# Performance work log

Measured on AMD Instinct MI355X. Metric: run time of the kernel, lower is better.

The kernel has to match this reference:

```python
import jax, jax.numpy as jnp
import numpy as np

EPS = 1e-6
B, T, J, D, H = 8, 512, 26, 256, 8
DH = D // H
HID = 4 * D


def logmap0(x):
    # x: [..., d+1] on hyperboloid (curvature -1). Tangent at origin -> [..., d]
    x0 = jnp.clip(x[..., :1], 1.0 + 1e-7, None)
    xs = x[..., 1:]
    n = jnp.maximum(jnp.linalg.norm(xs, axis=-1, keepdims=True), EPS)
    return jnp.arccosh(x0) * xs / n


def expmap0(v):
    # v: [..., d] tangent at origin -> [..., d+1] on hyperboloid
    n = jnp.maximum(jnp.linalg.norm(v, axis=-1, keepdims=True), EPS)
    return jnp.concatenate([jnp.cosh(n), jnp.sinh(n) * v / n], axis=-1)


def layernorm(v, g, b):
    m = jnp.mean(v, axis=-1, keepdims=True)
    var = jnp.var(v, axis=-1, keepdims=True)
    return (v - m) * jax.lax.rsqrt(var + 1e-5) * g + b


def lorentz_residual(x, z):
    # Lorentz centroid: normalize x+z so <m,m>_L = -1
    m = x + z
    mink = -m[..., :1] ** 2 + jnp.sum(m[..., 1:] ** 2, axis=-1, keepdims=True)
    return m / jnp.sqrt(jnp.clip(-mink, EPS, None))


def setup_inputs() -> dict:
    key = jax.random.key(0)
    ks = jax.random.split(key, 12)
    xs = jax.random.normal(ks[0], (B, T, J, D), jnp.float32) * 0.5
    x0 = jnp.sqrt(1.0 + jnp.sum(xs ** 2, axis=-1, keepdims=True))
    x = jnp.concatenate([x0, xs], axis=-1)  # valid points on H^d
    s = 1.0 / np.sqrt(D)
    inp = {
        "x": x,
        "g1": jnp.ones((D,), jnp.float32), "beta1": jnp.zeros((D,), jnp.float32),
        "Wq": jax.random.normal(ks[1], (D, D), jnp.float32) * s,
        "Wk": jax.random.normal(ks[2], (D, D), jnp.float32) * s,
        "Wv": jax.random.normal(ks[3], (D, D), jnp.float32) * s,
        "Wo": jax.random.normal(ks[4], (D, D), jnp.float32) * s,
        "bq": jnp.zeros((D,), jnp.float32), "bk": jnp.zeros((D,), jnp.float32),
        "bv": jnp.zeros((D,), jnp.float32), "bo": jnp.zeros((D,), jnp.float32),
        "g2": jnp.ones((D,), jnp.float32), "beta2": jnp.zeros((D,), jnp.float32),
        "W1": jax.random.normal(ks[5], (D, HID), jnp.float32) * s,
        "bf1": jnp.zeros((HID,), jnp.float32),
        "W2": jax.random.normal(ks[6], (HID, D), jnp.float32) * (1.0 / np.sqrt(HID)),
        "bf2": jnp.zeros((D,), jnp.float32),
    }
    return inp


def reference(x, g1, beta1, Wq, Wk, Wv, Wo, bq, bk, bv, bo, g2, beta2, W1, bf1, W2, bf2):
    # norm1: tangent-space LayerNorm
    u = layernorm(logmap0(x), g1, beta1)            # [B,T,J,D]
    xn = expmap0(u)
    # linear temporal attention (per joint, across T)
    t = logmap0(xn)
    q = (t @ Wq + bq).reshape(B, T, J, H, DH)
    k = (t @ Wk + bk).reshape(B, T, J, H, DH)
    v = (t @ Wv + bv).reshape(B, T, J, H, DH)
    pq = jax.nn.elu(q) + 1.0
    pk = jax.nn.elu(k) + 1.0
    kv = jnp.einsum('btjhk,btjhd->bjhkd', pk, v)    # O(T) global context
    ksum = jnp.sum(pk, axis=1)                      # [B,J,H,DH]
    num = jnp.einsum('btjhk,bjhkd->btjhd', pq, kv)
    den = jnp.einsum('btjhk,bjhk->btjh', pq, ksum)[..., None] + EPS
    o = (num / den).reshape(B, T, J, D) @ Wo + bo
    z = expmap0(o)
    # Lorentz (Minkowski) residual
    h = lorentz_residual(x, z)
    # norm2 + FFN in tangent space
    u2 = layernorm(logmap0(h), g2, beta2)
    f = jax.nn.gelu(u2 @ W1 + bf1) @ W2 + bf2
    return expmap0(f)
```

## Files before the change

### kernel.cpp

```cpp
#include <hip/hip_runtime.h>
#include <hip/hip_bf16.h>
#include <math.h>


#define EPSF 1e-6f
#define B_ 8
#define T_ 512
#define J_ 26
#define D_ 256
#define H_ 8
#define DH_ 32
#define HID_ 1024
#define NP1 257
#define R_ (B_*T_*J_)

typedef float  f32x4  __attribute__((ext_vector_type(4)));
typedef short  s16x8  __attribute__((ext_vector_type(8)));
typedef short  s16x4  __attribute__((ext_vector_type(4)));

__device__ __forceinline__ void async16(const void* g, void* l) {
  __builtin_amdgcn_global_load_lds(
      (const __attribute__((address_space(1))) unsigned int*)g,
      (__attribute__((address_space(3))) unsigned int*)l, 16, 0, 0);
}

__device__ __forceinline__ float wave_sum(float v) {
#pragma unroll
  for (int m = 32; m; m >>= 1) v += __shfl_xor(v, m, 64);
  return v;
}

__global__ __launch_bounds__(256) void k_wconv(const float* __restrict__ W,
                                               __hip_bfloat16* __restrict__ Wt,
                                               int K, int N) {
  __shared__ float tile[32][33];
  int n0 = blockIdx.x * 32, k0 = blockIdx.y * 32;
  int tx = threadIdx.x, ty = threadIdx.y;
#pragma unroll
  for (int i = ty; i < 32; i += 8) tile[i][tx] = W[(size_t)(k0 + i) * N + n0 + tx];
  __syncthreads();
#pragma unroll
  for (int i = ty; i < 32; i += 8)
    Wt[(size_t)(n0 + i) * K + k0 + tx] = __float2bfloat16(tile[tx][i]);
}

__global__ __launch_bounds__(256) void k_t(const float* __restrict__ x,
                                           const float* __restrict__ g1,
                                           const float* __restrict__ beta1,
                                           __hip_bfloat16* __restrict__ t) {
  int r = blockIdx.x * 4 + (threadIdx.x >> 6);
  int l = threadIdx.x & 63;
  const float* xr = x + (size_t)r * NP1;
  float xs[4];
#pragma unroll
  for (int i = 0; i < 4; ++i) xs[i] = xr[1 + l + 64*i];
  float p1 = xs[0]+xs[1]+xs[2]+xs[3];
  float p2 = xs[0]*xs[0]+xs[1]*xs[1]+xs[2]*xs[2]+xs[3]*xs[3];
  float s1 = wave_sum(p1);
  float s2 = wave_sum(p2);
  float mean = s1 * (1.0f/256.0f);
  float var = s2 * (1.0f/256.0f) - mean*mean;
  float rstd = rsqrtf(var + 1e-5f);
#pragma unroll
  for (int i = 0; i < 4; ++i) {
    int c = l + 64*i;
    t[(size_t)r * D_ + c] = __float2bfloat16((xs[i]-mean)*rstd*g1[c] + beta1[c]);
  }
}

#define PHASE(BUF, MH, NH, GIDX, DO_VM) {                                      \
    s16x8 af_[4][2]; s16x8 bf_[2][2];                                          \
    const char* ab_ = lds + ((BUF)*2+(MH))*16384;                              \
    const char* bb_ = lds + 65536 + ((BUF)*2+(NH))*16384;                      \
    _Pragma("unroll") for (int f_ = 0; f_ < 4; ++f_)                           \
      _Pragma("unroll") for (int ks_ = 0; ks_ < 2; ++ks_)                      \
        af_[f_][ks_] = *(const s16x8*)(ab_ + aoffs[f_][ks_]);                  \
    _Pragma("unroll") for (int ni_ = 0; ni_ < 2; ++ni_)                        \
      _Pragma("unroll") for (int ks_ = 0; ks_ < 2; ++ks_)                      \
        bf_[ni_][ks_] = *(const s16x8*)(bb_ + boffs[ni_][ks_]);                \
    STAGE_HALF((GIDX) + 6);                                                    \
    if (DO_VM) asm volatile("s_waitcnt vmcnt(4)" ::: "memory");                \
    asm volatile("s_barrier" ::: "memory");                                    \
    __builtin_amdgcn_sched_barrier(0);                                         \
    __builtin_amdgcn_s_setprio(1);                                             \
    _Pragma("unroll") for (int ks_ = 0; ks_ < 2; ++ks_)                        \
      _Pragma("unroll") for (int f_ = 0; f_ < 4; ++f_)                         \
        _Pragma("unroll") for (int ni_ = 0; ni_ < 2; ++ni_)                    \
          acc[(MH)*4+f_][(NH)*2+ni_] = __builtin_amdgcn_mfma_f32_16x16x32_bf16(\
              bf_[ni_][ks_], af_[f_][ks_], acc[(MH)*4+f_][(NH)*2+ni_], 0,0,0); \
    __builtin_amdgcn_s_setprio(0);                                             \
    asm volatile("s_barrier" ::: "memory");                                    \
  }

template<int ACT, int OUTF, int KDIM>
__global__ __launch_bounds__(512, 2) void k_gemm(const __hip_bfloat16* __restrict__ A,
                                                 const __hip_bfloat16* __restrict__ Bt,
                                                 const float* __restrict__ bias,
                                                 void* __restrict__ Cout,
                                                 int M, int N) {
  extern __shared__ char lds[];
  constexpr int NKT = KDIM / 64;
  int tid = threadIdx.x;
  int w = tid >> 6, l = tid & 63;
  int wr = w >> 2, wc = w & 3;
  int ml = l & 15, quad = l >> 4;
  int n0 = blockIdx.x * 256, m0 = blockIdx.y * 256;

  const short* Ag = (const short*)A + (size_t)m0 * KDIM;
  const short* Bg = (const short*)Bt + (size_t)n0 * KDIM;

  int srow = w*8 + (l >> 3);
  int scol = (((l & 7) ^ ((l >> 3) & 7)) * 8);

  auto STAGE_HALF = [&](int n) {
    if (n >= 4*NKT) return;
    int kt = n >> 2;
    int isB = n & 1, h = (n >> 1) & 1, buf = kt & 1;
    const short* src = isB ? Bg : Ag;
    const short* g0 = src + (size_t)(h*128 + srow) * KDIM + kt*64 + scol;
    char* dst = lds + isB*65536 + (buf*2 + h)*16384 + w*1024;
    async16(g0, dst);
    async16(g0 + (size_t)64 * KDIM, dst + 8192);
  };

  int aoffs[4][2], boffs[2][2];
#pragma unroll
  for (int f = 0; f < 4; ++f) {
    int r = wr*64 + f*16 + ml;
#pragma unroll
    for (int ks = 0; ks < 2; ++ks)
      aoffs[f][ks] = (r*128 + ks*64 + quad*16) ^ ((ml & 7) << 4);
  }
#pragma unroll
  for (int ni = 0; ni < 2; ++ni) {
    int rb = wc*32 + ni*16 + ml;
#pragma unroll
    for (int ks = 0; ks < 2; ++ks)
      boffs[ni][ks] = (rb*128 + ks*64 + quad*16) ^ ((ml & 7) << 4);
  }

  f32x4 acc[8][4];
#pragma unroll
  for (int i = 0; i < 8; ++i)
#pragma unroll
    for (int j = 0; j < 4; ++j) acc[i][j] = {0.f, 0.f, 0.f, 0.f};

#pragma unroll
  for (int n = 0; n < 6; ++n) STAGE_HALF(n);
  asm volatile("s_waitcnt vmcnt(4)" ::: "memory");
  asm volatile("s_barrier" ::: "memory");

  for (int cc = 0; cc < NKT/2; ++cc) {
    int g0 = cc * 8;
    PHASE(0, 0, 0, g0+0, 0)
    PHASE(0, 0, 1, g0+1, 0)
    PHASE(0, 1, 0, g0+2, 0)
    PHASE(0, 1, 1, g0+3, 1)
    PHASE(1, 0, 0, g0+4, 0)
    PHASE(1, 0, 1, g0+5, 0)
    PHASE(1, 1, 0, g0+6, 0)
    PHASE(1, 1, 1, g0+7, 1)
  }

#pragma unroll
  for (int mi = 0; mi < 8; ++mi) {
    size_t row = (size_t)(m0 + (mi>>2)*128 + wr*64 + (mi&3)*16 + ml);
#pragma unroll
    for (int nj = 0; nj < 4; ++nj) {
      int col = n0 + (nj>>1)*128 + wc*32 + (nj&1)*16 + quad*4;
      f32x4 bj = *(const f32x4*)&bias[col];
      f32x4 v = acc[mi][nj] + bj;
      if (ACT == 1) {
#pragma unroll
        for (int e = 0; e < 4; ++e) v[e] = (v[e] > 0.0f) ? v[e] + 1.0f : __expf(v[e]);
      } else if (ACT == 2) {
#pragma unroll
        for (int e = 0; e < 4; ++e) {
          float vv = v[e], v2 = vv * vv;
          float ex = __expf(vv * fmaf(v2, -0.0713548327f, -1.5957691216f));
          v[e] = vv * __builtin_amdgcn_rcpf(1.0f + ex);
        }
      }
      if (OUTF) {
        *(f32x4*)&((float*)Cout)[row * N + col] = v;
      } else {
        s16x4 sv;
#pragma unroll
        for (int e = 0; e < 4; ++e) {
          __hip_bfloat16 b = __float2bfloat16(v[e]);
          sv[e] = *(short*)&b;
        }
        *(s16x4*)&((__hip_bfloat16*)Cout)[row * N + col] = sv;
      }
    }
  }
}

__global__ __launch_bounds__(256) void k_kv(const __hip_bfloat16* __restrict__ pk,
                                            const __hip_bfloat16* __restrict__ v,
                                            float* __restrict__ kv,
                                            float* __restrict__ ksum) {
  __shared__ float spk[8][DH_];
  __shared__ float sv[8][DH_];
  int blk = blockIdx.x;
  int h = blk & 7;
  int bj = blk >> 3;
  int j = bj % J_;
  int b = bj / J_;
  int tid = threadIdx.x;
  int tt = tid >> 5, dl = tid & 31;
  int dd = tid & 31, k0 = tid >> 5;
  float acc[4] = {0.f, 0.f, 0.f, 0.f};
  float ks = 0.f;
  for (int t0 = 0; t0 < T_; t0 += 8) {
    size_t row = (size_t)(b * T_ + t0 + tt) * J_ + j;
    spk[tt][dl] = __bfloat162float(pk[row * D_ + h * DH_ + dl]);
    sv[tt][dl]  = __bfloat162float(v [row * D_ + h * DH_ + dl]);
    __syncthreads();
#pragma unroll
    for (int q = 0; q < 8; ++q) {
      float vv = sv[q][dd];
#pragma unroll
      for (int m = 0; m < 4; ++m)
        acc[m] = fmaf(spk[q][k0 + (m << 3)], vv, acc[m]);
    }
    if (tid < 32) {
#pragma unroll
      for (int q = 0; q < 8; ++q) ks += spk[q][tid];
    }
    __syncthreads();
  }
#pragma unroll
  for (int m = 0; m < 4; ++m)
    kv[(size_t)blk * (DH_*DH_) + (size_t)(k0 + (m << 3)) * DH_ + dd] = acc[m];
  if (tid < 32) ksum[(size_t)blk * DH_ + tid] = ks;
}

__global__ __launch_bounds__(256) void k_attn(const __hip_bfloat16* __restrict__ pq,
                                              const float* __restrict__ kv,
                                              const float* __restrict__ ksum,
                                              __hip_bfloat16* __restrict__ attn) {
  __shared__ float psf[32][264];
  __shared__ float dens[32][8];
  int bj = blockIdx.y;
  int b = bj / J_, j = bj % J_;
  int t0 = blockIdx.x * 32;
  int tid = threadIdx.x, w = tid >> 6, l = tid & 63;
  int h = w*2 + (l >> 5), dd = l & 31;

  const float* kvp = kv + ((size_t)bj * 8 + h) * (DH_*DH_);
  float kvreg[32];
#pragma unroll
  for (int k = 0; k < 32; ++k) kvreg[k] = kvp[k*32 + dd];

  for (int tr = 0; tr < 32; ++tr) {
    int g = (b * T_ + t0 + tr) * J_ + j;
    psf[tr][tid] = __bfloat162float(pq[(size_t)g * D_ + tid]);
  }
  __syncthreads();

  {
    int tr = tid & 31, hh = tid >> 5;
    const float* ksp = ksum + ((size_t)bj * 8 + hh) * DH_;
    float dsum = 0.f;
#pragma unroll
    for (int k = 0; k < 32; ++k) dsum = fmaf(psf[tr][hh*32 + k], ksp[k], dsum);
    dens[tr][hh] = dsum;
  }
  __syncthreads();

  for (int tr = 0; tr < 32; ++tr) {
    const float* pr = &psf[tr][h*32];
    float num = 0.f;
#pragma unroll
    for (int k = 0; k < 32; ++k) num = fmaf(pr[k], kvreg[k], num);
    int g = (b * T_ + t0 + tr) * J_ + j;
    float rden = __builtin_amdgcn_rcpf(dens[tr][h] + EPSF);
    attn[(size_t)g * D_ + tid] = __float2bfloat16(num * rden);
  }
}

__global__ __launch_bounds__(256) void k_u2(const __hip_bfloat16* __restrict__ o,
                                            const float* __restrict__ x,
                                            const float* __restrict__ g2,
                                            const float* __restrict__ beta2,
                                            __hip_bfloat16* __restrict__ u2) {
  int r = blockIdx.x * 4 + (threadIdx.x >> 6);
  int l = threadIdx.x & 63;
  const float* xr = x + (size_t)r * NP1;
  float ov[4], xs[4];
#pragma unroll
  for (int i = 0; i < 4; ++i) {
    ov[i] = __bfloat162float(o[(size_t)r * D_ + l + 64*i]);
    xs[i] = xr[1 + l + 64*i];
  }
  float p2 = ov[0]*ov[0]+ov[1]*ov[1]+ov[2]*ov[2]+ov[3]*ov[3];
  float s2o = wave_sum(p2);
  float no = fmaxf(sqrtf(s2o), EPSF);
  float e = __expf(no);
  float c = (e - 1.0f/e) * 0.5f / no;
  float mi[4];
#pragma unroll
  for (int i = 0; i < 4; ++i) mi[i] = xs[i] + c * ov[i];
  float q1 = mi[0]+mi[1]+mi[2]+mi[3];
  float q2 = mi[0]*mi[0]+mi[1]*mi[1]+mi[2]*mi[2]+mi[3]*mi[3];
  float s1 = wave_sum(q1);
  float s2 = wave_sum(q2);
  float mean = s1 * (1.0f/256.0f);
  float var = s2 * (1.0f/256.0f) - mean*mean;
  float rstd = rsqrtf(var + 1e-5f);
#pragma unroll
  for (int i = 0; i < 4; ++i) {
    int cc = l + 64*i;
    u2[(size_t)r * D_ + cc] = __float2bfloat16((mi[i]-mean)*rstd*g2[cc] + beta2[cc]);
  }
}

__global__ __launch_bounds__(256) void k_out(const float* __restrict__ f,
                                             float* __restrict__ out) {
  int r = blockIdx.x * 4 + (threadIdx.x >> 6);
  int l = threadIdx.x & 63;
  const float* fr = f + (size_t)r * D_;
  float fv[4];
#pragma unroll
  for (int i = 0; i < 4; ++i) fv[i] = fr[l + 64*i];
  float p2 = fv[0]*fv[0]+fv[1]*fv[1]+fv[2]*fv[2]+fv[3]*fv[3];
  float s2 = wave_sum(p2);
  float n = fmaxf(sqrtf(s2), EPSF);
  float e = __expf(n);
  float ie = 1.0f / e;
  float sh = (e - ie) * 0.5f;
  float ch = (e + ie) * 0.5f;
  float s = sh / n;
  float* orow = out + (size_t)r * NP1;
  if (l == 0) orow[0] = ch;
#pragma unroll
  for (int i = 0; i < 4; ++i) orow[1 + l + 64*i] = s * fv[i];
}

extern "C" void kernel_launch(void* const* d_in, const int* in_sizes, int n_in,
                              void* d_out, int out_size, void* d_ws, size_t ws_size,
                              hipStream_t stream) {
  const float* x     = (const float*)d_in[0];
  const float* g1    = (const float*)d_in[1];
  const float* beta1 = (const float*)d_in[2];
  const float* Wq    = (const float*)d_in[3];
  const float* Wk    = (const float*)d_in[4];
  const float* Wv    = (const float*)d_in[5];
  const float* Wo    = (const float*)d_in[6];
  const float* bq    = (const float*)d_in[7];
  const float* bk    = (const float*)d_in[8];
  const float* bv    = (const float*)d_in[9];
  const float* bo    = (const float*)d_in[10];
  const float* g2    = (const float*)d_in[11];
  const float* beta2 = (const float*)d_in[12];
  const float* W1    = (const float*)d_in[13];
  const float* bf1   = (const float*)d_in[14];
  const float* W2    = (const float*)d_in[15];
  const float* bf2   = (const float*)d_in[16];
  float* out = (float*)d_out;
  char* ws = (char*)d_ws;

  size_t off = 0;
  __hip_bfloat16* wqT = (__hip_bfloat16*)(ws + off); off += (size_t)D_*D_*2;
  __hip_bfloat16* wkT = (__hip_bfloat16*)(ws + off); off += (size_t)D_*D_*2;
  __hip_bfloat16* wvT = (__hip_bfloat16*)(ws + off); off += (size_t)D_*D_*2;
  __hip_bfloat16* woT = (__hip_bfloat16*)(ws + off); off += (size_t)D_*D_*2;
  __hip_bfloat16* w1T = (__hip_bfloat16*)(ws + off); off += (size_t)HID_*D_*2;
  __hip_bfloat16* w2T = (__hip_bfloat16*)(ws + off); off += (size_t)D_*HID_*2;
  float* kvb = (float*)(ws + off); off += (size_t)(B_*J_*H_)*(DH_*DH_)*4;
  float* ksb = (float*)(ws + off); off += (size_t)(B_*J_*H_)*DH_*4;
  off = (off + 255) & ~(size_t)255;
  __hip_bfloat16* tb = (__hip_bfloat16*)(ws + off); off += (size_t)R_*D_*2;
  __hip_bfloat16* qb = (__hip_bfloat16*)(ws + off); off += (size_t)R_*D_*2;
  __hip_bfloat16* kb = (__hip_bfloat16*)(ws + off); off += (size_t)R_*D_*2;
  __hip_bfloat16* vb = (__hip_bfloat16*)(ws + off); off += (size_t)R_*D_*2;
  __hip_bfloat16* hid = (__hip_bfloat16*)(ws + off); off += (size_t)(R_/2)*HID_*2;
  float* fbuf = (float*)qb;

  static bool attr_done = false;
  if (!attr_done) {
    hipFuncSetAttribute((const void*)k_gemm<1,0,256>,  hipFuncAttributeMaxDynamicSharedMemorySize, 131072);
    hipFuncSetAttribute((const void*)k_gemm<0,0,256>,  hipFuncAttributeMaxDynamicSharedMemorySize, 131072);
    hipFuncSetAttribute((const void*)k_gemm<2,0,256>,  hipFuncAttributeMaxDynamicSharedMemorySize, 131072);
    hipFuncSetAttribute((const void*)k_gemm<0,1,1024>, hipFuncAttributeMaxDynamicSharedMemorySize, 131072);
    attr_done = true;
  }

  dim3 tconv(32, 8);
  k_wconv<<<dim3(D_/32,  D_/32),  tconv, 0, stream>>>(Wq, wqT, D_,  D_);
  k_wconv<<<dim3(D_/32,  D_/32),  tconv, 0, stream>>>(Wk, wkT, D_,  D_);
  k_wconv<<<dim3(D_/32,  D_/32),  tconv, 0, stream>>>(Wv, wvT, D_,  D_);
  k_wconv<<<dim3(D_/32,  D_/32),  tconv, 0, stream>>>(Wo, woT, D_,  D_);
  k_wconv<<<dim3(HID_/32, D_/32), tconv, 0, stream>>>(W1, w1T, D_,  HID_);
  k_wconv<<<dim3(D_/32, HID_/32), tconv, 0, stream>>>(W2, w2T, HID_, D_);

  k_t<<<R_/4, 256, 0, stream>>>(x, g1, beta1, tb);

  dim3 gqkv(D_/256, R_/256);
  k_gemm<1,0,256><<<gqkv, 512, 131072, stream>>>(tb, wqT, bq, qb, R_, D_);
  k_gemm<1,0,256><<<gqkv, 512, 131072, stream>>>(tb, wkT, bk, kb, R_, D_);
  k_gemm<0,0,256><<<gqkv, 512, 131072, stream>>>(tb, wvT, bv, vb, R_, D_);

  k_kv<<<B_*J_*H_, 256, 0, stream>>>(kb, vb, kvb, ksb);
  k_attn<<<dim3(T_/32, B_*J_), 256, 0, stream>>>(qb, kvb, ksb, kb);

  k_gemm<0,0,256><<<gqkv, 512, 131072, stream>>>(kb, woT, bo, vb, R_, D_);
  k_u2<<<R_/4, 256, 0, stream>>>(vb, x, g2, beta2, tb);

  const int Rc = R_ / 2;
  for (int c = 0; c < 2; ++c) {
    k_gemm<2,0,256><<<dim3(HID_/256, Rc/256), 512, 131072, stream>>>(
        tb + (size_t)c * Rc * D_, w1T, bf1, hid, Rc, HID_);
    k_gemm<0,1,1024><<<dim3(D_/256, Rc/256), 512, 131072, stream>>>(
        hid, w2T, bf2, fbuf + (size_t)c * Rc * D_, Rc, D_);
  }

  k_out<<<R_/4, 256, 0, stream>>>(fbuf, out);
}
```

Baseline: 802.4 us.

## Permute intermediate rows to (b,j,t) order and double-buffer kv reduction

Intermediate activations are now stored in (batch, joint, time) row order instead of (batch, time, joint). The row permutation is applied at the entry kernel and undone at the output kernel. This makes the per-joint temporal reductions in k_kv and k_attn read contiguous rows instead of rows strided by the joint count. k_kv is also rewritten to load 64 timesteps per chunk with vector loads into double-buffered shared memory, with fewer barriers. The input and output row-wise kernels now read and write x and out through a gathered index, and the GEMMs are assumed to be row-order agnostic.

```diff
diff --git a/kernel.cpp b/kernel.cpp
--- a/kernel.cpp
+++ b/kernel.cpp
@@ -18,6 +18,12 @@
 typedef short  s16x8  __attribute__((ext_vector_type(8)));
 typedef short  s16x4  __attribute__((ext_vector_type(4)));
 
+__device__ __forceinline__ int rp_to_r(int rp) {
+  int bj = rp >> 9, t = rp & 511;
+  int b = bj / 26, j = bj - 26 * b;
+  return (b * 512 + t) * 26 + j;
+}
+
 __device__ __forceinline__ void async16(const void* g, void* l) {
   __builtin_amdgcn_global_load_lds(
       (const __attribute__((address_space(1))) unsigned int*)g,
@@ -48,8 +54,9 @@
                                            const float* __restrict__ g1,
                                            const float* __restrict__ beta1,
                                            __hip_bfloat16* __restrict__ t) {
-  int r = blockIdx.x * 4 + (threadIdx.x >> 6);
+  int rp = blockIdx.x * 4 + (threadIdx.x >> 6);
   int l = threadIdx.x & 63;
+  int r = rp_to_r(rp);
   const float* xr = x + (size_t)r * NP1;
   float xs[4];
 #pragma unroll
@@ -64,7 +71,7 @@
 #pragma unroll
   for (int i = 0; i < 4; ++i) {
     int c = l + 64*i;
-    t[(size_t)r * D_ + c] = __float2bfloat16((xs[i]-mean)*rstd*g1[c] + beta1[c]);
+    t[(size_t)rp * D_ + c] = __float2bfloat16((xs[i]-mean)*rstd*g1[c] + beta1[c]);
   }
 }
 
@@ -200,40 +207,78 @@
                                             const __hip_bfloat16* __restrict__ v,
                                             float* __restrict__ kv,
                                             float* __restrict__ ksum) {
-  __shared__ float spk[8][DH_];
-  __shared__ float sv[8][DH_];
+  __shared__ float spk[2][64*36];
+  __shared__ float sv [2][64*33];
+  __shared__ float sks[8][32];
   int blk = blockIdx.x;
-  int h = blk & 7;
-  int bj = blk >> 3;
-  int j = bj % J_;
-  int b = bj / J_;
+  int h = blk & 7, bj = blk >> 3;
   int tid = threadIdx.x;
-  int tt = tid >> 5, dl = tid & 31;
-  int dd = tid & 31, k0 = tid >> 5;
+  int tq = tid >> 2;
+  int qc = tid & 3;
+  int kgrp = tid >> 5;
+  int dd = tid & 31;
+
+  const short* pkg = (const short*)pk + (size_t)bj * 512 * 256 + h*32 + qc*8;
+  const short* vg  = (const short*)v  + (size_t)bj * 512 * 256 + h*32 + qc*8;
+
   float acc[4] = {0.f, 0.f, 0.f, 0.f};
   float ks = 0.f;
-  for (int t0 = 0; t0 < T_; t0 += 8) {
-    size_t row = (size_t)(b * T_ + t0 + tt) * J_ + j;
-    spk[tt][dl] = __bfloat162float(pk[row * D_ + h * DH_ + dl]);
-    sv[tt][dl]  = __bfloat162float(v [row * D_ + h * DH_ + dl]);
+  s16x8 rp_, rv_;
+
+  auto GLOAD = [&](int c) {
+    size_t off = (size_t)(c*64 + tq) * 256;
+    rp_ = *(const s16x8*)(pkg + off);
+    rv_ = *(const s16x8*)(vg + off);
+  };
+  auto DSWRITE = [&](int c) {
+    int bsel = c & 1;
+    float* prow = &spk[bsel][tq*36];
+    float* vrow = &sv[bsel][tq*33];
+#pragma unroll
+    for (int e = 0; e < 8; ++e) {
+      unsigned up = ((unsigned)(unsigned short)rp_[e]) << 16;
+      unsigned uv = ((unsigned)(unsigned short)rv_[e]) << 16;
+      prow[e*4 + qc]  = __uint_as_float(up);
+      vrow[qc*8 + e]  = __uint_as_float(uv);
+    }
+  };
+  auto COMPUTE = [&](int c) {
+    int bsel = c & 1;
+    const float* pb = &spk[bsel][kgrp*4];
+    const float* vb = &sv[bsel][dd];
+#pragma unroll
+    for (int t = 0; t < 64; ++t) {
+      f32x4 pf = *(const f32x4*)(pb + t*36);
+      float vv = vb[t*33];
+#pragma unroll
+      for (int m = 0; m < 4; ++m) acc[m] = fmaf(pf[m], vv, acc[m]);
+    }
+    const float* kb = &spk[bsel][kgrp*8*36 + ((dd&7)<<2) + (dd>>3)];
+#pragma unroll
+    for (int i = 0; i < 8; ++i) ks += kb[i*36];
+  };
+
+  GLOAD(0);
+#pragma unroll 2
+  for (int c = 0; c < 8; ++c) {
+    DSWRITE(c);
+    if (c < 7) GLOAD(c + 1);
     __syncthreads();
-#pragma unroll
-    for (int q = 0; q < 8; ++q) {
-      float vv = sv[q][dd];
-#pragma unroll
-      for (int m = 0; m < 4; ++m)
-        acc[m] = fmaf(spk[q][k0 + (m << 3)], vv, acc[m]);
-    }
-    if (tid < 32) {
-#pragma unroll
-      for (int q = 0; q < 8; ++q) ks += spk[q][tid];
-    }
-    __syncthreads();
-  }
-#pragma unroll
-  for (int m = 0; m < 4; ++m)
-    kv[(size_t)blk * (DH_*DH_) + (size_t)(k0 + (m << 3)) * DH_ + dd] = acc[m];
-  if (tid < 32) ksum[(size_t)blk * DH_ + tid] = ks;
+    COMPUTE(c);
+  }
+
+  float* kvp = kv + (size_t)blk * 1024;
+#pragma unroll
+  for (int m = 0; m < 4; ++m) kvp[(kgrp + 8*m)*32 + dd] = acc[m];
+
+  sks[kgrp][dd] = ks;
+  __syncthreads();
+  if (tid < 32) {
+    float s = 0.f;
+#pragma unroll
+    for (int g = 0; g < 8; ++g) s += sks[g][tid];
+    ksum[(size_t)blk * 32 + tid] = s;
+  }
 }
 
 __global__ __launch_bounds__(256) void k_attn(const __hip_bfloat16* __restrict__ pq,
@@ -243,8 +288,8 @@
   __shared__ float psf[32][264];
   __shared__ float dens[32][8];
   int bj = blockIdx.y;
-  int b = bj / J_, j = bj % J_;
   int t0 = blockIdx.x * 32;
+  int g0 = bj * 512 + t0;
   int tid = threadIdx.x, w = tid >> 6, l = tid & 63;
   int h = w*2 + (l >> 5), dd = l & 31;
 
@@ -253,10 +298,8 @@
 #pragma unroll
   for (int k = 0; k < 32; ++k) kvreg[k] = kvp[k*32 + dd];
 
-  for (int tr = 0; tr < 32; ++tr) {
-    int g = (b * T_ + t0 + tr) * J_ + j;
-    psf[tr][tid] = __bfloat162float(pq[(size_t)g * D_ + tid]);
-  }
+  for (int tr = 0; tr < 32; ++tr)
+    psf[tr][tid] = __bfloat162float(pq[(size_t)(g0 + tr) * D_ + tid]);
   __syncthreads();
 
   {
@@ -274,9 +317,8 @@
     float num = 0.f;
 #pragma unroll
     for (int k = 0; k < 32; ++k) num = fmaf(pr[k], kvreg[k], num);
-    int g = (b * T_ + t0 + tr) * J_ + j;
     float rden = __builtin_amdgcn_rcpf(dens[tr][h] + EPSF);
-    attn[(size_t)g * D_ + tid] = __float2bfloat16(num * rden);
+    attn[(size_t)(g0 + tr) * D_ + tid] = __float2bfloat16(num * rden);
   }
 }
 
@@ -285,13 +327,14 @@
                                             const float* __restrict__ g2,
                                             const float* __restrict__ beta2,
                                             __hip_bfloat16* __restrict__ u2) {
-  int r = blockIdx.x * 4 + (threadIdx.x >> 6);
+  int rp = blockIdx.x * 4 + (threadIdx.x >> 6);
   int l = threadIdx.x & 63;
+  int r = rp_to_r(rp);
   const float* xr = x + (size_t)r * NP1;
   float ov[4], xs[4];
 #pragma unroll
   for (int i = 0; i < 4; ++i) {
-    ov[i] = __bfloat162float(o[(size_t)r * D_ + l + 64*i]);
+    ov[i] = __bfloat162float(o[(size_t)rp * D_ + l + 64*i]);
     xs[i] = xr[1 + l + 64*i];
   }
   float p2 = ov[0]*ov[0]+ov[1]*ov[1]+ov[2]*ov[2]+ov[3]*ov[3];
@@ -312,15 +355,16 @@
 #pragma unroll
   for (int i = 0; i < 4; ++i) {
     int cc = l + 64*i;
-    u2[(size_t)r * D_ + cc] = __float2bfloat16((mi[i]-mean)*rstd*g2[cc] + beta2[cc]);
+    u2[(size_t)rp * D_ + cc] = __float2bfloat16((mi[i]-mean)*rstd*g2[cc] + beta2[cc]);
   }
 }
 
 __global__ __launch_bounds__(256) void k_out(const float* __restrict__ f,
                                              float* __restrict__ out) {
-  int r = blockIdx.x * 4 + (threadIdx.x >> 6);
+  int rp = blockIdx.x * 4 + (threadIdx.x >> 6);
   int l = threadIdx.x & 63;
-  const float* fr = f + (size_t)r * D_;
+  int r = rp_to_r(rp);
+  const float* fr = f + (size_t)rp * D_;
   float fv[4];
 #pragma unroll
   for (int i = 0; i < 4; ++i) fv[i] = fr[l + 64*i];
```

Result: no change. 802.7 us (+0.0%).
